# Kernel tuning notes

Hardware: AMD Instinct MI355X
Metric: run time of the kernel (lower is better)

The kernel has to match this reference:

```python
import jax, jax.numpy as jnp
import numpy as np

N_RAYS = 8192
N_SAMPLES = 128
HIDDEN = 128
SH_DIM = 16
RAY_EXT_FACTOR = 10.0


def rsh_cart_3(d):
    # Real spherical harmonics up to degree 3, Cartesian form (16 coeffs).
    x, y, z = d[..., 0], d[..., 1], d[..., 2]
    x2, y2, z2 = x * x, y * y, z * z
    xy, yz, xz = x * y, y * z, x * z
    return jnp.stack([
        0.282094791773878 * jnp.ones_like(x),
        -0.48860251190292 * y,
        0.48860251190292 * z,
        -0.48860251190292 * x,
        1.0925484305920792 * xy,
        -1.0925484305920792 * yz,
        0.94617469575756 * z2 - 0.31539156525252,
        -1.0925484305920792 * xz,
        0.5462742152960396 * (x2 - y2),
        0.5900435899266435 * y * (-3.0 * x2 + y2),
        2.8906114426405538 * xy * z,
        0.4570457994644658 * y * (1.0 - 5.0 * z2),
        0.3731763325901154 * z * (5.0 * z2 - 3.0),
        0.4570457994644658 * x * (1.0 - 5.0 * z2),
        1.445305721320277 * z * (x2 - y2),
        0.5900435899266435 * x * (-x2 + 3.0 * y2),
    ], axis=-1)


def setup_inputs() -> dict:
    key = jax.random.key(0)
    ks = jax.random.split(key, 11)
    o = jax.random.normal(ks[0], (N_RAYS, 3), dtype=jnp.float32)
    origins = 2.5 * o / jnp.linalg.norm(o, axis=-1, keepdims=True)
    # aim roughly at the unit AABB so most rays are active
    dirs = -origins + 0.2 * jax.random.normal(ks[1], (N_RAYS, 3), dtype=jnp.float32)
    u = jax.random.uniform(ks[2], (N_RAYS, N_SAMPLES), dtype=jnp.float32)
    s1 = 1.0 / np.sqrt(3.0)
    s2 = 1.0 / np.sqrt(HIDDEN)
    s3 = 1.0 / np.sqrt(HIDDEN + SH_DIM)
    return {
        'origins': origins,
        'dirs': dirs,
        'u': u,
        'W1': s1 * jax.random.normal(ks[3], (3, HIDDEN), dtype=jnp.float32),
        'b1': jnp.zeros((HIDDEN,), jnp.float32),
        'W2': s2 * jax.random.normal(ks[4], (HIDDEN, HIDDEN), dtype=jnp.float32),
        'b2': jnp.zeros((HIDDEN,), jnp.float32),
        'Wd': s2 * jax.random.normal(ks[5], (HIDDEN, 1), dtype=jnp.float32),
        'bd': jnp.zeros((1,), jnp.float32),
        'Wc': s3 * jax.random.normal(ks[6], (HIDDEN + SH_DIM, 3), dtype=jnp.float32),
        'bc': jnp.zeros((3,), jnp.float32),
    }


def reference(origins, dirs, u, W1, b1, W2, b2, Wd, bd, Wc, bc):
    B, T = u.shape
    # ---- AABB ([-1,1]^3) slab intersection -> tnear/tfar, active mask ----
    inv_d = 1.0 / dirs
    t1 = (-1.0 - origins) * inv_d
    t2 = (1.0 - origins) * inv_d
    tnear = jnp.maximum(jnp.max(jnp.minimum(t1, t2), axis=-1), 0.0)  # (B,)
    tfar = jnp.min(jnp.maximum(t1, t2), axis=-1)                      # (B,)
    active = tfar > tnear                                             # (B,)
    tfar_c = jnp.maximum(tfar, tnear + 1e-3)
    # ---- stratified ray step sampling ----
    frac = (jnp.arange(T, dtype=u.dtype) + u) / T                     # (B,T)
    ts = tnear[:, None] + (tfar_c - tnear)[:, None] * frac            # (B,T)
    xyz = origins[:, None, :] + dirs[:, None, :] * ts[..., None]      # (B,T,3)
    # aabb is [-1,1]^3 so ndc == xyz; spatial filter = bounds test
    xyz_ndc = xyz
    mask = jnp.all(jnp.abs(xyz_ndc) <= 1.0, axis=-1) & active[:, None]  # (B,T)
    dnorm = jnp.linalg.norm(dirs, axis=-1)                            # (B,)
    ynm = rsh_cart_3(dirs / dnorm[:, None])                           # (B,16)
    # ---- radiance field MLP over all sample points ----
    x = xyz_ndc.reshape(B * T, 3)
    h = jax.nn.relu(x @ W1 + b1)
    h = jax.nn.relu(h @ W2 + b2)
    sigma = jax.nn.softplus(h @ Wd + bd).reshape(B, T)
    cond = jnp.broadcast_to(ynm[:, None, :], (B, T, SH_DIM)).reshape(B * T, SH_DIM)
    color = jax.nn.sigmoid(jnp.concatenate([h, cond], axis=-1) @ Wc + bc).reshape(B, T, 3)
    # zero out points rejected by the spatial filter (torch writes only masked)
    sigma = sigma * mask
    color = color * mask[..., None]
    # ---- transmittance integration (integrate_timesteps) ----
    tfinal = tfar_c * RAY_EXT_FACTOR
    deltas = jnp.diff(ts, axis=-1, append=tfinal[:, None])            # (B,T)
    sd = sigma * deltas * dnorm[:, None]
    csum = jnp.cumsum(sd, axis=-1)
    # weights_i = T_i * alpha_i = exp(-csum_{i-1}) - exp(-csum_i)
    weights = jnp.exp(sd - csum) - jnp.exp(-csum)                     # (B,T)
    color_out = jnp.einsum('bt,btc->bc', weights, color)              # (B,3)
    alpha_out = jnp.sum(weights, axis=-1, keepdims=True)              # (B,1)
    rgba = jnp.concatenate([color_out, alpha_out], axis=-1)           # (B,4)
    return jnp.where(active[:, None], rgba, 0.0)
```

## Files before the change

kernel.cpp:

```cpp
#include <hip/hip_runtime.h>
#include <math.h>

#define NRAYS 8192
#define T 128
#define H 128
#define SHD 16

using short8 = __attribute__((ext_vector_type(8))) short;
using f32x4  = __attribute__((ext_vector_type(4))) float;
using f32x2  = __attribute__((ext_vector_type(2))) float;
using u32x2  = __attribute__((ext_vector_type(2))) unsigned;

__device__ __forceinline__ float fexp(float x) {
  return exp2f(x * 1.44269504088896341f);
}
__device__ __forceinline__ float softplus_f(float x) {
  return fmaxf(x, 0.f) + 0.693147180559945309f * log2f(1.f + fexp(-fabsf(x)));
}
__device__ __forceinline__ float sigmoid_f(float x) {
  return __builtin_amdgcn_rcpf(1.f + fexp(-x));
}

__device__ __forceinline__ unsigned f2bf(float f) {
  unsigned u = __float_as_uint(f);
  return (u + 0x7fffu + ((u >> 16) & 1u)) >> 16;
}

__device__ __forceinline__ unsigned pk2(f32x2 h) {
  const u32x2 u = __builtin_bit_cast(u32x2, h) + (u32x2){0x8000u, 0x8000u};
  return __builtin_amdgcn_perm(u[1], u[0], 0x07060302u);
}

__global__ void preprocess(const float* __restrict__ W2, const float* __restrict__ Wd,
                           const float* __restrict__ Wc,
                           unsigned short* __restrict__ w2t,
                           unsigned short* __restrict__ woutf) {
  const int t = blockIdx.x * 256 + threadIdx.x;
  if (t < 16384) {
    const int n = t >> 7, p = t & 127;
    const int o = (p >> 3) ^ (n & 7);
    const int k = o * 8 + (p & 7);
    w2t[t] = (unsigned short)f2bf(W2[k * 128 + n]);
  }
  if (t < 2048) {
    const int kk = t >> 9, L = (t >> 3) & 63, j = t & 7;
    const int c = L & 15, g = L >> 4;
    const int k = kk * 32 + g * 8 + j;
    float v = 0.f;
    if (c == 0) v = Wd[k];
    else if (c < 4) v = Wc[k * 3 + (c - 1)];
    woutf[t] = (unsigned short)f2bf(v);
  }
}

__global__ __launch_bounds__(256, 4) void nerf_render(
    const float* __restrict__ origins, const float* __restrict__ dirs,
    const float* __restrict__ u, const float* __restrict__ W1,
    const float* __restrict__ b1, const float* __restrict__ b2,
    const float* __restrict__ bd, const float* __restrict__ Wc,
    const float* __restrict__ bc, const unsigned short* __restrict__ w2t,
    const unsigned short* __restrict__ woutf, float* __restrict__ out)
{
  const int ray = blockIdx.x;
  const int tid = threadIdx.x;
  const int L = tid & 63;
  const int w = tid >> 6;
  const int g = L >> 4;
  const int c = L & 15;

  __shared__ __align__(16) short Bs[16384];
  __shared__ __align__(16) short As2[4 * 640];
  __shared__ __align__(16) float baseA[H];
  __shared__ __align__(16) float slopeA[H];
  __shared__ float ts_s[T];
  __shared__ float mask_s[T];
  __shared__ float rayp[8];
  __shared__ float wred[2][4];
  __shared__ float wtot[2];

  {
    const float4* src = (const float4*)w2t;
    float4* dst = (float4*)Bs;
    #pragma unroll
    for (int i = 0; i < 8; ++i) dst[tid + i * 256] = src[tid + i * 256];
  }

  if (tid < T) {
    const int tl = tid;
    const float ox = origins[ray*3+0], oy = origins[ray*3+1], oz = origins[ray*3+2];
    const float dx = dirs[ray*3+0],  dy = dirs[ray*3+1],  dz = dirs[ray*3+2];
    const float ix = 1.f/dx, iy = 1.f/dy, iz = 1.f/dz;
    const float t1x = (-1.f-ox)*ix, t2x = (1.f-ox)*ix;
    const float t1y = (-1.f-oy)*iy, t2y = (1.f-oy)*iy;
    const float t1z = (-1.f-oz)*iz, t2z = (1.f-oz)*iz;
    float tnear = fmaxf(fmaxf(fminf(t1x,t2x), fminf(t1y,t2y)), fminf(t1z,t2z));
    tnear = fmaxf(tnear, 0.f);
    const float tfar = fminf(fminf(fmaxf(t1x,t2x), fmaxf(t1y,t2y)), fmaxf(t1z,t2z));
    const bool  active = tfar > tnear;
    const float tfar_c = fmaxf(tfar, tnear + 1e-3f);
    const float ut = u[ray*T + tl];
    const float frac = ((float)tl + ut) * (1.f/(float)T);
    const float tt = tnear + (tfar_c - tnear) * frac;
    const float px = fmaf(dx, tt, ox);
    const float py = fmaf(dy, tt, oy);
    const float pz = fmaf(dz, tt, oz);
    ts_s[tl] = tt;
    const bool m = (fabsf(px) <= 1.f) && (fabsf(py) <= 1.f) && (fabsf(pz) <= 1.f) && active;
    mask_s[tl] = m ? 1.f : 0.f;
    const float w0 = W1[tl], w1v = W1[H + tl], w2v = W1[2*H + tl];
    baseA[tl]  = fmaf(ox, w0, fmaf(oy, w1v, fmaf(oz, w2v, b1[tl])));
    slopeA[tl] = fmaf(dx, w0, fmaf(dy, w1v, dz * w2v));
    if (tl == 0) {
      rayp[0] = tfar_c;
      rayp[1] = sqrtf(dx*dx + dy*dy + dz*dz);
      rayp[2] = active ? 1.f : 0.f;
    }
  } else if (tid == 128) {
    const float dx = dirs[ray*3+0], dy = dirs[ray*3+1], dz = dirs[ray*3+2];
    const float dnorm = sqrtf(dx*dx + dy*dy + dz*dz);
    const float nx = dx/dnorm, ny = dy/dnorm, nz = dz/dnorm;
    const float x2 = nx*nx, y2 = ny*ny, z2 = nz*nz;
    const float xy = nx*ny, yz = ny*nz, xz = nx*nz;
    float ynm[16];
    ynm[0]  = 0.282094791773878f;
    ynm[1]  = -0.48860251190292f*ny;
    ynm[2]  = 0.48860251190292f*nz;
    ynm[3]  = -0.48860251190292f*nx;
    ynm[4]  = 1.0925484305920792f*xy;
    ynm[5]  = -1.0925484305920792f*yz;
    ynm[6]  = 0.94617469575756f*z2 - 0.31539156525252f;
    ynm[7]  = -1.0925484305920792f*xz;
    ynm[8]  = 0.5462742152960396f*(x2-y2);
    ynm[9]  = 0.5900435899266435f*ny*(-3.f*x2+y2);
    ynm[10] = 2.8906114426405538f*xy*nz;
    ynm[11] = 0.4570457994644658f*ny*(1.f-5.f*z2);
    ynm[12] = 0.3731763325901154f*nz*(5.f*z2-3.f);
    ynm[13] = 0.4570457994644658f*nx*(1.f-5.f*z2);
    ynm[14] = 1.445305721320277f*nz*(x2-y2);
    ynm[15] = 0.5900435899266435f*nx*(-x2+3.f*y2);
    float cp0 = bc[0], cp1 = bc[1], cp2 = bc[2];
    #pragma unroll
    for (int s = 0; s < SHD; ++s) {
      cp0 = fmaf(ynm[s], Wc[(H+s)*3+0], cp0);
      cp1 = fmaf(ynm[s], Wc[(H+s)*3+1], cp1);
      cp2 = fmaf(ynm[s], Wc[(H+s)*3+2], cp2);
    }
    rayp[3] = cp0; rayp[4] = cp1; rayp[5] = cp2;
  }

  f32x4 acc[2][8];
  #pragma unroll
  for (int mt = 0; mt < 8; ++mt) {
    const float4 bv = *(const float4*)&b2[mt*16 + g*4];
    #pragma unroll
    for (int tm = 0; tm < 2; ++tm) {
      acc[tm][mt][0] = bv.x; acc[tm][mt][1] = bv.y;
      acc[tm][mt][2] = bv.z; acc[tm][mt][3] = bv.w;
    }
  }
  __syncthreads();

  const float t0 = ts_s[32*w + c];
  const float t1 = ts_s[32*w + 16 + c];
  const f32x2 tz0 = {t0, t0}, tz1 = {t1, t1};
  const f32x2 zero2 = {0.f, 0.f};

  #pragma unroll
  for (int ks = 0; ks < 4; ++ks) {
    const int kb = ks*32 + g*8;
    const f32x4 bq0 = *(const f32x4*)&baseA[kb];
    const f32x4 bq1 = *(const f32x4*)&baseA[kb+4];
    const f32x4 sq0 = *(const f32x4*)&slopeA[kb];
    const f32x4 sq1 = *(const f32x4*)&slopeA[kb+4];
    const f32x2 b01 = {bq0[0], bq0[1]}, b23 = {bq0[2], bq0[3]};
    const f32x2 b45 = {bq1[0], bq1[1]}, b67 = {bq1[2], bq1[3]};
    const f32x2 s01 = {sq0[0], sq0[1]}, s23 = {sq0[2], sq0[3]};
    const f32x2 s45 = {sq1[0], sq1[1]}, s67 = {sq1[2], sq1[3]};
    const f32x2 a01 = __builtin_elementwise_max(__builtin_elementwise_fma(tz0, s01, b01), zero2);
    const f32x2 a23 = __builtin_elementwise_max(__builtin_elementwise_fma(tz0, s23, b23), zero2);
    const f32x2 a45 = __builtin_elementwise_max(__builtin_elementwise_fma(tz0, s45, b45), zero2);
    const f32x2 a67 = __builtin_elementwise_max(__builtin_elementwise_fma(tz0, s67, b67), zero2);
    const f32x2 e01 = __builtin_elementwise_max(__builtin_elementwise_fma(tz1, s01, b01), zero2);
    const f32x2 e23 = __builtin_elementwise_max(__builtin_elementwise_fma(tz1, s23, b23), zero2);
    const f32x2 e45 = __builtin_elementwise_max(__builtin_elementwise_fma(tz1, s45, b45), zero2);
    const f32x2 e67 = __builtin_elementwise_max(__builtin_elementwise_fma(tz1, s67, b67), zero2);
    union U { uint4 u; short8 s; } A0, A1;
    A0.u = make_uint4(pk2(a01), pk2(a23), pk2(a45), pk2(a67));
    A1.u = make_uint4(pk2(e01), pk2(e23), pk2(e45), pk2(e67));
    const int swb = ((ks*4 + g) ^ (c & 7)) * 8;
    #pragma unroll
    for (int mt = 0; mt < 8; ++mt) {
      const short8 wf = *(const short8*)&Bs[(mt*16 + c)*128 + swb];
      acc[0][mt] = __builtin_amdgcn_mfma_f32_16x16x32_bf16(wf, A0.s, acc[0][mt], 0, 0, 0);
      acc[1][mt] = __builtin_amdgcn_mfma_f32_16x16x32_bf16(wf, A1.s, acc[1][mt], 0, 0, 0);
    }
  }
  __syncthreads();
  float4* SredP = (float4*)Bs;

  short* As2w = As2 + w * 640;
  short8 wa[4];
  #pragma unroll
  for (int kk = 0; kk < 4; ++kk)
    wa[kk] = *(const short8*)&woutf[(kk*64 + L)*8];

  #pragma unroll
  for (int tm = 0; tm < 2; ++tm) {
    f32x4 oacc;
    oacc[0] = 0.f; oacc[1] = 0.f; oacc[2] = 0.f; oacc[3] = 0.f;
    #pragma unroll
    for (int kk = 0; kk < 4; ++kk) {
      #pragma unroll
      for (int i = 0; i < 2; ++i) {
        const f32x4 a = acc[tm][kk*2 + i];
        const f32x2 h01 = __builtin_elementwise_max((f32x2){a[0], a[1]}, zero2);
        const f32x2 h23 = __builtin_elementwise_max((f32x2){a[2], a[3]}, zero2);
        *(uint2*)&As2w[c*40 + i*16 + g*4] = make_uint2(pk2(h01), pk2(h23));
      }
      const short8 hbf = *(const short8*)&As2w[c*40 + g*8];
      oacc = __builtin_amdgcn_mfma_f32_16x16x32_bf16(wa[kk], hbf, oacc, 0, 0, 0);
    }
    if (g == 0)
      SredP[32*w + 16*tm + c] = make_float4(oacc[0], oacc[1], oacc[2], oacc[3]);
  }
  __syncthreads();

  float sd = 0.f, cc0 = 0.f, cc1 = 0.f, cc2 = 0.f;
  if (tid < T) {
    const float4 sv = SredP[tid];
    const float mk = mask_s[tid];
    const float sigma = softplus_f(sv.x + bd[0]) * mk;
    cc0 = mk * sigmoid_f(sv.y + rayp[3]);
    cc1 = mk * sigmoid_f(sv.z + rayp[4]);
    cc2 = mk * sigmoid_f(sv.w + rayp[5]);
    const float tt = ts_s[tid];
    const float tnext = (tid < T-1) ? ts_s[tid + 1] : rayp[0] * 10.f;
    sd = sigma * (tnext - tt) * rayp[1];
  }

  float val = sd;
  #pragma unroll
  for (int off = 1; off < 64; off <<= 1) {
    const float tmp = __shfl_up(val, off);
    if (L >= off) val += tmp;
  }
  if (tid < T && L == 63) wtot[w] = val;
  __syncthreads();
  const float csum = val + ((w == 1) ? wtot[0] : 0.f);

  float wgt = 0.f, wcx = 0.f, wcy = 0.f, wcz = 0.f;
  if (tid < T) {
    wgt = fexp(sd - csum) - fexp(-csum);
    wcx = wgt * cc0; wcy = wgt * cc1; wcz = wgt * cc2;
  }
  #pragma unroll
  for (int mm = 32; mm >= 1; mm >>= 1) {
    wgt += __shfl_xor(wgt, mm);
    wcx += __shfl_xor(wcx, mm);
    wcy += __shfl_xor(wcy, mm);
    wcz += __shfl_xor(wcz, mm);
  }
  if (tid < T && L == 0) {
    wred[w][0] = wgt; wred[w][1] = wcx; wred[w][2] = wcy; wred[w][3] = wcz;
  }
  __syncthreads();
  if (tid == 0) {
    const float aw = wred[0][0] + wred[1][0];
    const float o0 = wred[0][1] + wred[1][1];
    const float o1 = wred[0][2] + wred[1][2];
    const float o2 = wred[0][3] + wred[1][3];
    const bool act = rayp[2] != 0.f;
    out[ray*4+0] = act ? o0 : 0.f;
    out[ray*4+1] = act ? o1 : 0.f;
    out[ray*4+2] = act ? o2 : 0.f;
    out[ray*4+3] = act ? aw : 0.f;
  }
}

extern "C" void kernel_launch(void* const* d_in, const int* in_sizes, int n_in,
                              void* d_out, int out_size, void* d_ws, size_t ws_size,
                              hipStream_t stream) {
  const float* origins = (const float*)d_in[0];
  const float* dirs    = (const float*)d_in[1];
  const float* u       = (const float*)d_in[2];
  const float* W1      = (const float*)d_in[3];
  const float* b1      = (const float*)d_in[4];
  const float* W2      = (const float*)d_in[5];
  const float* b2      = (const float*)d_in[6];
  const float* Wd      = (const float*)d_in[7];
  const float* bd      = (const float*)d_in[8];
  const float* Wc      = (const float*)d_in[9];
  const float* bc      = (const float*)d_in[10];

  unsigned short* w2t   = (unsigned short*)d_ws;
  unsigned short* woutf = (unsigned short*)((char*)d_ws + 32768);

  preprocess<<<64, 256, 0, stream>>>(W2, Wd, Wc, w2t, woutf);
  nerf_render<<<NRAYS, 256, 0, stream>>>(origins, dirs, u, W1, b1, b2, bd, Wc, bc,
                                         w2t, woutf, (float*)d_out);
}
```

Before: 135.0 us.

## Process four rays per block to amortize W2 staging into LDS

Each block now loops over four rays and loads the bf16 W2 tile into shared memory once, instead of every block reloading it for a single ray. The load uses direct global-to-LDS transfers. Because the weight buffer now stays live across rays, the output-reduction scratch moves from the weight buffer to the As2 buffer, and an extra barrier closes each ray iteration. The cost is a quarter as many blocks and rays handled serially within a block, which lowers available parallelism and tail balance.

```diff
diff --git a/kernel.cpp b/kernel.cpp
--- a/kernel.cpp
+++ b/kernel.cpp
@@ -5,6 +5,8 @@
 #define T 128
 #define H 128
 #define SHD 16
+#define RPL 4
+#define NBLK (NRAYS / RPL)
 
 using short8 = __attribute__((ext_vector_type(8))) short;
 using f32x4  = __attribute__((ext_vector_type(4))) float;
@@ -29,6 +31,12 @@
 __device__ __forceinline__ unsigned pk2(f32x2 h) {
   const u32x2 u = __builtin_bit_cast(u32x2, h) + (u32x2){0x8000u, 0x8000u};
   return __builtin_amdgcn_perm(u[1], u[0], 0x07060302u);
+}
+
+__device__ __forceinline__ void gload_lds16(const void* g, void* l) {
+  __builtin_amdgcn_global_load_lds(
+      (const __attribute__((address_space(1))) unsigned*)g,
+      (__attribute__((address_space(3))) unsigned*)l, 16, 0, 0);
 }
 
 __global__ void preprocess(const float* __restrict__ W2, const float* __restrict__ Wd,
@@ -61,7 +69,6 @@
     const float* __restrict__ bc, const unsigned short* __restrict__ w2t,
     const unsigned short* __restrict__ woutf, float* __restrict__ out)
 {
-  const int ray = blockIdx.x;
   const int tid = threadIdx.x;
   const int L = tid & 63;
   const int w = tid >> 6;
@@ -78,202 +85,212 @@
   __shared__ float wred[2][4];
   __shared__ float wtot[2];
 
-  {
-    const float4* src = (const float4*)w2t;
-    float4* dst = (float4*)Bs;
-    #pragma unroll
-    for (int i = 0; i < 8; ++i) dst[tid + i * 256] = src[tid + i * 256];
+  #pragma unroll
+  for (int i = 0; i < 8; ++i) {
+    const int idx = (i * 256 + tid) * 8;
+    gload_lds16(&w2t[idx], &Bs[idx]);
   }
 
-  if (tid < T) {
-    const int tl = tid;
-    const float ox = origins[ray*3+0], oy = origins[ray*3+1], oz = origins[ray*3+2];
-    const float dx = dirs[ray*3+0],  dy = dirs[ray*3+1],  dz = dirs[ray*3+2];
-    const float ix = 1.f/dx, iy = 1.f/dy, iz = 1.f/dz;
-    const float t1x = (-1.f-ox)*ix, t2x = (1.f-ox)*ix;
-    const float t1y = (-1.f-oy)*iy, t2y = (1.f-oy)*iy;
-    const float t1z = (-1.f-oz)*iz, t2z = (1.f-oz)*iz;
-    float tnear = fmaxf(fmaxf(fminf(t1x,t2x), fminf(t1y,t2y)), fminf(t1z,t2z));
-    tnear = fmaxf(tnear, 0.f);
-    const float tfar = fminf(fminf(fmaxf(t1x,t2x), fmaxf(t1y,t2y)), fmaxf(t1z,t2z));
-    const bool  active = tfar > tnear;
-    const float tfar_c = fmaxf(tfar, tnear + 1e-3f);
-    const float ut = u[ray*T + tl];
-    const float frac = ((float)tl + ut) * (1.f/(float)T);
-    const float tt = tnear + (tfar_c - tnear) * frac;
-    const float px = fmaf(dx, tt, ox);
-    const float py = fmaf(dy, tt, oy);
-    const float pz = fmaf(dz, tt, oz);
-    ts_s[tl] = tt;
-    const bool m = (fabsf(px) <= 1.f) && (fabsf(py) <= 1.f) && (fabsf(pz) <= 1.f) && active;
-    mask_s[tl] = m ? 1.f : 0.f;
-    const float w0 = W1[tl], w1v = W1[H + tl], w2v = W1[2*H + tl];
-    baseA[tl]  = fmaf(ox, w0, fmaf(oy, w1v, fmaf(oz, w2v, b1[tl])));
-    slopeA[tl] = fmaf(dx, w0, fmaf(dy, w1v, dz * w2v));
-    if (tl == 0) {
-      rayp[0] = tfar_c;
-      rayp[1] = sqrtf(dx*dx + dy*dy + dz*dz);
-      rayp[2] = active ? 1.f : 0.f;
-    }
-  } else if (tid == 128) {
-    const float dx = dirs[ray*3+0], dy = dirs[ray*3+1], dz = dirs[ray*3+2];
-    const float dnorm = sqrtf(dx*dx + dy*dy + dz*dz);
-    const float nx = dx/dnorm, ny = dy/dnorm, nz = dz/dnorm;
-    const float x2 = nx*nx, y2 = ny*ny, z2 = nz*nz;
-    const float xy = nx*ny, yz = ny*nz, xz = nx*nz;
-    float ynm[16];
-    ynm[0]  = 0.282094791773878f;
-    ynm[1]  = -0.48860251190292f*ny;
-    ynm[2]  = 0.48860251190292f*nz;
-    ynm[3]  = -0.48860251190292f*nx;
-    ynm[4]  = 1.0925484305920792f*xy;
-    ynm[5]  = -1.0925484305920792f*yz;
-    ynm[6]  = 0.94617469575756f*z2 - 0.31539156525252f;
-    ynm[7]  = -1.0925484305920792f*xz;
-    ynm[8]  = 0.5462742152960396f*(x2-y2);
-    ynm[9]  = 0.5900435899266435f*ny*(-3.f*x2+y2);
-    ynm[10] = 2.8906114426405538f*xy*nz;
-    ynm[11] = 0.4570457994644658f*ny*(1.f-5.f*z2);
-    ynm[12] = 0.3731763325901154f*nz*(5.f*z2-3.f);
-    ynm[13] = 0.4570457994644658f*nx*(1.f-5.f*z2);
-    ynm[14] = 1.445305721320277f*nz*(x2-y2);
-    ynm[15] = 0.5900435899266435f*nx*(-x2+3.f*y2);
-    float cp0 = bc[0], cp1 = bc[1], cp2 = bc[2];
-    #pragma unroll
-    for (int s = 0; s < SHD; ++s) {
-      cp0 = fmaf(ynm[s], Wc[(H+s)*3+0], cp0);
-      cp1 = fmaf(ynm[s], Wc[(H+s)*3+1], cp1);
-      cp2 = fmaf(ynm[s], Wc[(H+s)*3+2], cp2);
-    }
-    rayp[3] = cp0; rayp[4] = cp1; rayp[5] = cp2;
-  }
-
-  f32x4 acc[2][8];
-  #pragma unroll
-  for (int mt = 0; mt < 8; ++mt) {
-    const float4 bv = *(const float4*)&b2[mt*16 + g*4];
+  for (int rr = 0; rr < RPL; ++rr) {
+    const int ray = blockIdx.x * RPL + rr;
+
+    if (tid < T) {
+      const int tl = tid;
+      const float ox = origins[ray*3+0], oy = origins[ray*3+1], oz = origins[ray*3+2];
+      const float dx = dirs[ray*3+0],  dy = dirs[ray*3+1],  dz = dirs[ray*3+2];
+      const float ix = 1.f/dx, iy = 1.f/dy, iz = 1.f/dz;
+      const float t1x = (-1.f-ox)*ix, t2x = (1.f-ox)*ix;
+      const float t1y = (-1.f-oy)*iy, t2y = (1.f-oy)*iy;
+      const float t1z = (-1.f-oz)*iz, t2z = (1.f-oz)*iz;
+      float tnear = fmaxf(fmaxf(fminf(t1x,t2x), fminf(t1y,t2y)), fminf(t1z,t2z));
+      tnear = fmaxf(tnear, 0.f);
+      const float tfar = fminf(fminf(fmaxf(t1x,t2x), fmaxf(t1y,t2y)), fmaxf(t1z,t2z));
+      const bool  active = tfar > tnear;
+      const float tfar_c = fmaxf(tfar, tnear + 1e-3f);
+      const float ut = u[ray*T + tl];
+      const float frac = ((float)tl + ut) * (1.f/(float)T);
+      const float tt = tnear + (tfar_c - tnear) * frac;
+      const float px = fmaf(dx, tt, ox);
+      const float py = fmaf(dy, tt, oy);
+      const float pz = fmaf(dz, tt, oz);
+      ts_s[tl] = tt;
+      const bool m = (fabsf(px) <= 1.f) && (fabsf(py) <= 1.f) && (fabsf(pz) <= 1.f) && active;
+      mask_s[tl] = m ? 1.f : 0.f;
+      const float w0 = W1[tl], w1v = W1[H + tl], w2v = W1[2*H + tl];
+      baseA[tl]  = fmaf(ox, w0, fmaf(oy, w1v, fmaf(oz, w2v, b1[tl])));
+      slopeA[tl] = fmaf(dx, w0, fmaf(dy, w1v, dz * w2v));
+      if (tl == 0) {
+        rayp[0] = tfar_c;
+        rayp[1] = sqrtf(dx*dx + dy*dy + dz*dz);
+        rayp[2] = active ? 1.f : 0.f;
+      }
+    } else if (tid == 128) {
+      const float dx = dirs[ray*3+0], dy = dirs[ray*3+1], dz = dirs[ray*3+2];
+      const float dnorm = sqrtf(dx*dx + dy*dy + dz*dz);
+      const float nx = dx/dnorm, ny = dy/dnorm, nz = dz/dnorm;
+      const float x2 = nx*nx, y2 = ny*ny, z2 = nz*nz;
+      const float xy = nx*ny, yz = ny*nz, xz = nx*nz;
+      float ynm[16];
+      ynm[0]  = 0.282094791773878f;
+      ynm[1]  = -0.48860251190292f*ny;
+      ynm[2]  = 0.48860251190292f*nz;
+      ynm[3]  = -0.48860251190292f*nx;
+      ynm[4]  = 1.0925484305920792f*xy;
+      ynm[5]  = -1.0925484305920792f*yz;
+      ynm[6]  = 0.94617469575756f*z2 - 0.31539156525252f;
+      ynm[7]  = -1.0925484305920792f*xz;
+      ynm[8]  = 0.5462742152960396f*(x2-y2);
+      ynm[9]  = 0.5900435899266435f*ny*(-3.f*x2+y2);
+      ynm[10] = 2.8906114426405538f*xy*nz;
+      ynm[11] = 0.4570457994644658f*ny*(1.f-5.f*z2);
+      ynm[12] = 0.3731763325901154f*nz*(5.f*z2-3.f);
+      ynm[13] = 0.4570457994644658f*nx*(1.f-5.f*z2);
+      ynm[14] = 1.445305721320277f*nz*(x2-y2);
+      ynm[15] = 0.5900435899266435f*nx*(-x2+3.f*y2);
+      float cp0 = bc[0], cp1 = bc[1], cp2 = bc[2];
+      #pragma unroll
+      for (int s = 0; s < SHD; ++s) {
+        cp0 = fmaf(ynm[s], Wc[(H+s)*3+0], cp0);
+        cp1 = fmaf(ynm[s], Wc[(H+s)*3+1], cp1);
+        cp2 = fmaf(ynm[s], Wc[(H+s)*3+2], cp2);
+      }
+      rayp[3] = cp0; rayp[4] = cp1; rayp[5] = cp2;
+    }
+
+    f32x4 acc[2][8];
+    #pragma unroll
+    for (int mt = 0; mt < 8; ++mt) {
+      const float4 bv = *(const float4*)&b2[mt*16 + g*4];
+      #pragma unroll
+      for (int tm = 0; tm < 2; ++tm) {
+        acc[tm][mt][0] = bv.x; acc[tm][mt][1] = bv.y;
+        acc[tm][mt][2] = bv.z; acc[tm][mt][3] = bv.w;
+      }
+    }
+    __syncthreads();
+
+    const float t0 = ts_s[32*w + c];
+    const float t1 = ts_s[32*w + 16 + c];
+    const f32x2 tz0 = {t0, t0}, tz1 = {t1, t1};
+    const f32x2 zero2 = {0.f, 0.f};
+
+    #pragma unroll
+    for (int ks = 0; ks < 4; ++ks) {
+      const int kb = ks*32 + g*8;
+      const f32x4 bq0 = *(const f32x4*)&baseA[kb];
+      const f32x4 bq1 = *(const f32x4*)&baseA[kb+4];
+      const f32x4 sq0 = *(const f32x4*)&slopeA[kb];
+      const f32x4 sq1 = *(const f32x4*)&slopeA[kb+4];
+      const f32x2 b01 = {bq0[0], bq0[1]}, b23 = {bq0[2], bq0[3]};
+      const f32x2 b45 = {bq1[0], bq1[1]}, b67 = {bq1[2], bq1[3]};
+      const f32x2 s01 = {sq0[0], sq0[1]}, s23 = {sq0[2], sq0[3]};
+      const f32x2 s45 = {sq1[0], sq1[1]}, s67 = {sq1[2], sq1[3]};
+      const f32x2 a01 = __builtin_elementwise_max(__builtin_elementwise_fma(tz0, s01, b01), zero2);
+      const f32x2 a23 = __builtin_elementwise_max(__builtin_elementwise_fma(tz0, s23, b23), zero2);
+      const f32x2 a45 = __builtin_elementwise_max(__builtin_elementwise_fma(tz0, s45, b45), zero2);
+      const f32x2 a67 = __builtin_elementwise_max(__builtin_elementwise_fma(tz0, s67, b67), zero2);
+      const f32x2 e01 = __builtin_elementwise_max(__builtin_elementwise_fma(tz1, s01, b01), zero2);
+      const f32x2 e23 = __builtin_elementwise_max(__builtin_elementwise_fma(tz1, s23, b23), zero2);
+      const f32x2 e45 = __builtin_elementwise_max(__builtin_elementwise_fma(tz1, s45, b45), zero2);
+      const f32x2 e67 = __builtin_elementwise_max(__builtin_elementwise_fma(tz1, s67, b67), zero2);
+      union U { uint4 u; short8 s; } A0, A1;
+      A0.u = make_uint4(pk2(a01), pk2(a23), pk2(a45), pk2(a67));
+      A1.u = make_uint4(pk2(e01), pk2(e23), pk2(e45), pk2(e67));
+      const int swb = ((ks*4 + g) ^ (c & 7)) * 8;
+      #pragma unroll
+      for (int mt = 0; mt < 8; ++mt) {
+        const short8 wf = *(const short8*)&Bs[(mt*16 + c)*128 + swb];
+        acc[0][mt] = __builtin_amdgcn_mfma_f32_16x16x32_bf16(wf, A0.s, acc[0][mt], 0, 0, 0);
+        acc[1][mt] = __builtin_amdgcn_mfma_f32_16x16x32_bf16(wf, A1.s, acc[1][mt], 0, 0, 0);
+      }
+    }
+
+    short* As2w = As2 + w * 640;
+    short8 wa[4];
+    #pragma unroll
+    for (int kk = 0; kk < 4; ++kk)
+      wa[kk] = *(const short8*)&woutf[(kk*64 + L)*8];
+
+    f32x4 osig[2];
     #pragma unroll
     for (int tm = 0; tm < 2; ++tm) {
-      acc[tm][mt][0] = bv.x; acc[tm][mt][1] = bv.y;
-      acc[tm][mt][2] = bv.z; acc[tm][mt][3] = bv.w;
-    }
-  }
-  __syncthreads();
-
-  const float t0 = ts_s[32*w + c];
-  const float t1 = ts_s[32*w + 16 + c];
-  const f32x2 tz0 = {t0, t0}, tz1 = {t1, t1};
-  const f32x2 zero2 = {0.f, 0.f};
-
-  #pragma unroll
-  for (int ks = 0; ks < 4; ++ks) {
-    const int kb = ks*32 + g*8;
-    const f32x4 bq0 = *(const f32x4*)&baseA[kb];
-    const f32x4 bq1 = *(const f32x4*)&baseA[kb+4];
-    const f32x4 sq0 = *(const f32x4*)&slopeA[kb];
-    const f32x4 sq1 = *(const f32x4*)&slopeA[kb+4];
-    const f32x2 b01 = {bq0[0], bq0[1]}, b23 = {bq0[2], bq0[3]};
-    const f32x2 b45 = {bq1[0], bq1[1]}, b67 = {bq1[2], bq1[3]};
-    const f32x2 s01 = {sq0[0], sq0[1]}, s23 = {sq0[2], sq0[3]};
-    const f32x2 s45 = {sq1[0], sq1[1]}, s67 = {sq1[2], sq1[3]};
-    const f32x2 a01 = __builtin_elementwise_max(__builtin_elementwise_fma(tz0, s01, b01), zero2);
-    const f32x2 a23 = __builtin_elementwise_max(__builtin_elementwise_fma(tz0, s23, b23), zero2);
-    const f32x2 a45 = __builtin_elementwise_max(__builtin_elementwise_fma(tz0, s45, b45), zero2);
-    const f32x2 a67 = __builtin_elementwise_max(__builtin_elementwise_fma(tz0, s67, b67), zero2);
-    const f32x2 e01 = __builtin_elementwise_max(__builtin_elementwise_fma(tz1, s01, b01), zero2);
-    const f32x2 e23 = __builtin_elementwise_max(__builtin_elementwise_fma(tz1, s23, b23), zero2);
-    const f32x2 e45 = __builtin_elementwise_max(__builtin_elementwise_fma(tz1, s45, b45), zero2);
-    const f32x2 e67 = __builtin_elementwise_max(__builtin_elementwise_fma(tz1, s67, b67), zero2);
-    union U { uint4 u; short8 s; } A0, A1;
-    A0.u = make_uint4(pk2(a01), pk2(a23), pk2(a45), pk2(a67));
-    A1.u = make_uint4(pk2(e01), pk2(e23), pk2(e45), pk2(e67));
-    const int swb = ((ks*4 + g) ^ (c & 7)) * 8;
-    #pragma unroll
-    for (int mt = 0; mt < 8; ++mt) {
-      const short8 wf = *(const short8*)&Bs[(mt*16 + c)*128 + swb];
-      acc[0][mt] = __builtin_amdgcn_mfma_f32_16x16x32_bf16(wf, A0.s, acc[0][mt], 0, 0, 0);
-      acc[1][mt] = __builtin_amdgcn_mfma_f32_16x16x32_bf16(wf, A1.s, acc[1][mt], 0, 0, 0);
-    }
-  }
-  __syncthreads();
-  float4* SredP = (float4*)Bs;
-
-  short* As2w = As2 + w * 640;
-  short8 wa[4];
-  #pragma unroll
-  for (int kk = 0; kk < 4; ++kk)
-    wa[kk] = *(const short8*)&woutf[(kk*64 + L)*8];
-
-  #pragma unroll
-  for (int tm = 0; tm < 2; ++tm) {
-    f32x4 oacc;
-    oacc[0] = 0.f; oacc[1] = 0.f; oacc[2] = 0.f; oacc[3] = 0.f;
-    #pragma unroll
-    for (int kk = 0; kk < 4; ++kk) {
-      #pragma unroll
-      for (int i = 0; i < 2; ++i) {
-        const f32x4 a = acc[tm][kk*2 + i];
-        const f32x2 h01 = __builtin_elementwise_max((f32x2){a[0], a[1]}, zero2);
-        const f32x2 h23 = __builtin_elementwise_max((f32x2){a[2], a[3]}, zero2);
-        *(uint2*)&As2w[c*40 + i*16 + g*4] = make_uint2(pk2(h01), pk2(h23));
-      }
-      const short8 hbf = *(const short8*)&As2w[c*40 + g*8];
-      oacc = __builtin_amdgcn_mfma_f32_16x16x32_bf16(wa[kk], hbf, oacc, 0, 0, 0);
-    }
-    if (g == 0)
-      SredP[32*w + 16*tm + c] = make_float4(oacc[0], oacc[1], oacc[2], oacc[3]);
-  }
-  __syncthreads();
-
-  float sd = 0.f, cc0 = 0.f, cc1 = 0.f, cc2 = 0.f;
-  if (tid < T) {
-    const float4 sv = SredP[tid];
-    const float mk = mask_s[tid];
-    const float sigma = softplus_f(sv.x + bd[0]) * mk;
-    cc0 = mk * sigmoid_f(sv.y + rayp[3]);
-    cc1 = mk * sigmoid_f(sv.z + rayp[4]);
-    cc2 = mk * sigmoid_f(sv.w + rayp[5]);
-    const float tt = ts_s[tid];
-    const float tnext = (tid < T-1) ? ts_s[tid + 1] : rayp[0] * 10.f;
-    sd = sigma * (tnext - tt) * rayp[1];
-  }
-
-  float val = sd;
-  #pragma unroll
-  for (int off = 1; off < 64; off <<= 1) {
-    const float tmp = __shfl_up(val, off);
-    if (L >= off) val += tmp;
-  }
-  if (tid < T && L == 63) wtot[w] = val;
-  __syncthreads();
-  const float csum = val + ((w == 1) ? wtot[0] : 0.f);
-
-  float wgt = 0.f, wcx = 0.f, wcy = 0.f, wcz = 0.f;
-  if (tid < T) {
-    wgt = fexp(sd - csum) - fexp(-csum);
-    wcx = wgt * cc0; wcy = wgt * cc1; wcz = wgt * cc2;
-  }
-  #pragma unroll
-  for (int mm = 32; mm >= 1; mm >>= 1) {
-    wgt += __shfl_xor(wgt, mm);
-    wcx += __shfl_xor(wcx, mm);
-    wcy += __shfl_xor(wcy, mm);
-    wcz += __shfl_xor(wcz, mm);
-  }
-  if (tid < T && L == 0) {
-    wred[w][0] = wgt; wred[w][1] = wcx; wred[w][2] = wcy; wred[w][3] = wcz;
-  }
-  __syncthreads();
-  if (tid == 0) {
-    const float aw = wred[0][0] + wred[1][0];
-    const float o0 = wred[0][1] + wred[1][1];
-    const float o1 = wred[0][2] + wred[1][2];
-    const float o2 = wred[0][3] + wred[1][3];
-    const bool act = rayp[2] != 0.f;
-    out[ray*4+0] = act ? o0 : 0.f;
-    out[ray*4+1] = act ? o1 : 0.f;
-    out[ray*4+2] = act ? o2 : 0.f;
-    out[ray*4+3] = act ? aw : 0.f;
+      f32x4 oacc;
+      oacc[0] = 0.f; oacc[1] = 0.f; oacc[2] = 0.f; oacc[3] = 0.f;
+      #pragma unroll
+      for (int kk = 0; kk < 4; ++kk) {
+        const f32x2 zz = {0.f, 0.f};
+        #pragma unroll
+        for (int i = 0; i < 2; ++i) {
+          const f32x4 a = acc[tm][kk*2 + i];
+          const f32x2 h01 = __builtin_elementwise_max((f32x2){a[0], a[1]}, zz);
+          const f32x2 h23 = __builtin_elementwise_max((f32x2){a[2], a[3]}, zz);
+          *(uint2*)&As2w[c*40 + i*16 + g*4] = make_uint2(pk2(h01), pk2(h23));
+        }
+        const short8 hbf = *(const short8*)&As2w[c*40 + g*8];
+        oacc = __builtin_amdgcn_mfma_f32_16x16x32_bf16(wa[kk], hbf, oacc, 0, 0, 0);
+      }
+      osig[tm] = oacc;
+    }
+    __syncthreads();
+    float4* SredA = (float4*)As2;
+    if (g == 0) {
+      #pragma unroll
+      for (int tm = 0; tm < 2; ++tm)
+        SredA[32*w + 16*tm + c] = make_float4(osig[tm][0], osig[tm][1], osig[tm][2], osig[tm][3]);
+    }
+    __syncthreads();
+
+    float sd = 0.f, cc0 = 0.f, cc1 = 0.f, cc2 = 0.f;
+    if (tid < T) {
+      const float4 sv = SredA[tid];
+      const float mk = mask_s[tid];
+      const float sigma = softplus_f(sv.x + bd[0]) * mk;
+      cc0 = mk * sigmoid_f(sv.y + rayp[3]);
+      cc1 = mk * sigmoid_f(sv.z + rayp[4]);
+      cc2 = mk * sigmoid_f(sv.w + rayp[5]);
+      const float tt = ts_s[tid];
+      const float tnext = (tid < T-1) ? ts_s[tid + 1] : rayp[0] * 10.f;
+      sd = sigma * (tnext - tt) * rayp[1];
+    }
+
+    float val = sd;
+    #pragma unroll
+    for (int off = 1; off < 64; off <<= 1) {
+      const float tmp = __shfl_up(val, off);
+      if (L >= off) val += tmp;
+    }
+    if (tid < T && L == 63) wtot[w] = val;
+    __syncthreads();
+    const float csum = val + ((w == 1) ? wtot[0] : 0.f);
+
+    float wgt = 0.f, wcx = 0.f, wcy = 0.f, wcz = 0.f;
+    if (tid < T) {
+      wgt = fexp(sd - csum) - fexp(-csum);
+      wcx = wgt * cc0; wcy = wgt * cc1; wcz = wgt * cc2;
+    }
+    #pragma unroll
+    for (int mm = 32; mm >= 1; mm >>= 1) {
+      wgt += __shfl_xor(wgt, mm);
+      wcx += __shfl_xor(wcx, mm);
+      wcy += __shfl_xor(wcy, mm);
+      wcz += __shfl_xor(wcz, mm);
+    }
+    if (tid < T && L == 0) {
+      wred[w][0] = wgt; wred[w][1] = wcx; wred[w][2] = wcy; wred[w][3] = wcz;
+    }
+    __syncthreads();
+    if (tid == 0) {
+      const float aw = wred[0][0] + wred[1][0];
+      const float o0 = wred[0][1] + wred[1][1];
+      const float o1 = wred[0][2] + wred[1][2];
+      const float o2 = wred[0][3] + wred[1][3];
+      const bool act = rayp[2] != 0.f;
+      out[ray*4+0] = act ? o0 : 0.f;
+      out[ray*4+1] = act ? o1 : 0.f;
+      out[ray*4+2] = act ? o2 : 0.f;
+      out[ray*4+3] = act ? aw : 0.f;
+    }
+    __syncthreads();
   }
 }
 
@@ -296,6 +313,6 @@
   unsigned short* woutf = (unsigned short*)((char*)d_ws + 32768);
 
   preprocess<<<64, 256, 0, stream>>>(W2, Wd, Wc, w2t, woutf);
-  nerf_render<<<NRAYS, 256, 0, stream>>>(origins, dirs, u, W1, b1, b2, bd, Wc, bc,
-                                         w2t, woutf, (float*)d_out);
-}
+  nerf_render<<<NBLK, 256, 0, stream>>>(origins, dirs, u, W1, b1, b2, bd, Wc, bc,
+                                        w2t, woutf, (float*)d_out);
+}
```

New measurement: 192.1 us. 1.42x slower.
